# Kernel tuning notes

Hardware: AMD Instinct MI355X
Metric: run time of the kernel (lower is better)

Reference implementation:

```python
import jax, jax.numpy as jnp
import numpy as np

DIAG = 64          # dynamic_mask_scale: |i-j| >= DIAG is masked
NEG_INF = float('-inf')

def _band_mask(L, diagonal):
    # True where masked out: j >= i + diagonal or i >= j + diagonal  <=>  |i-j| >= diagonal
    i = jnp.arange(L)[:, None]
    j = jnp.arange(L)[None, :]
    return jnp.abs(i - j) >= diagonal  # [L, L] bool

def setup_inputs() -> dict:
    key = jax.random.key(0)
    k1, k2, k3, k4 = jax.random.split(key, 4)
    B, L, H, E = 2, 2048, 8, 64
    queries = jax.random.normal(k1, (B, L, H, E), dtype=jnp.float32)
    keys = jax.random.normal(k2, (B, L, H, E), dtype=jnp.float32)
    values = jax.random.normal(k3, (B, L, H, E), dtype=jnp.float32)
    sigma = jax.random.normal(k4, (B, L, H), dtype=jnp.float32)
    attn_mask = jnp.zeros((B, 1, L, L), dtype=bool)  # unused (dynamic mask path)
    return {"queries": queries, "keys": keys, "values": values,
            "sigma": sigma, "attn_mask": attn_mask}

def reference(queries, keys, values, sigma, attn_mask):
    B, L, H, E = queries.shape
    scale = 1.0 / jnp.sqrt(jnp.float32(E))
    # scores: [B, H, L, S]
    scores = jnp.einsum('blhe,bshe->bhls', queries, keys)
    mask = _band_mask(L, DIAG)  # [L, L]
    scores = jnp.where(mask[None, None, :, :], NEG_INF, scores)
    attn = scale * scores
    series = jax.nn.softmax(attn, axis=-1)  # dropout p=0 -> identity
    V = jnp.einsum('bhls,bshd->blhd', series, values)
    return (V, series)
```

## Files before the change

### kernel.cpp

```cpp
#include <hip/hip_runtime.h>
#include <cstdint>

#define BB    2
#define LL    2048
#define HH    8
#define EE    64
#define DIAG  64
#define BAND  127
#define RR    16
#define TILE  143
#define SK    68
#define NT    256

__global__ __launch_bounds__(NT, 3) void anomaly_attn_kernel(
    const float* __restrict__ Q,
    const float* __restrict__ K,
    const float* __restrict__ V,
    float* __restrict__ outV,
    float* __restrict__ outS)
{
    __shared__ float lds_kv[TILE * SK];
    __shared__ float lds_s[RR * 128];
    __shared__ float lds_q[RR * EE];

    const int bid  = blockIdx.x;
    const int gblk = (bid & 7) * 256 + (bid >> 3);
    const int rb   = gblk & 127;
    const int h    = (gblk >> 7) & 7;
    const int b    = gblk >> 10;
    const int i0   = rb * RR;

    const int t    = threadIdx.x;
    const int wave = t >> 6;
    const int lane = t & 63;

    const size_t headOff = ((size_t)b * LL * HH + h) * EE;
    const int    rowStr  = HH * EE;

    {
        const int qrow = t >> 4, qf = t & 15;
        ((float4*)lds_q)[t] =
            *(const float4*)(Q + headOff + (size_t)(i0 + qrow) * rowStr + qf * 4);

        for (int idx = t; idx < TILE * 16; idx += NT) {
            const int trow = idx >> 4, tf = idx & 15;
            int j = i0 - (DIAG - 1) + trow;
            j = j < 0 ? 0 : (j > LL - 1 ? LL - 1 : j);
            float4 kv = *(const float4*)(K + headOff + (size_t)j * rowStr + tf * 4);
            *(float4*)(lds_kv + trow * SK + tf * 4) = kv;
        }
    }
    __syncthreads();

    const float scale = 0.125f;
    for (int r4 = 0; r4 < 4; ++r4) {
        const int r = wave * 4 + r4;
        const int i = i0 + r;
        const float* qrow = lds_q + r * EE;
        const float* k1   = lds_kv + (r + lane) * SK;
        const float* k2   = k1 + 64 * SK;
        float s1 = 0.f, s2 = 0.f;
#pragma unroll
        for (int c = 0; c < 16; ++c) {
            const float4 q4 = *(const float4*)(qrow + c * 4);
            const float4 a4 = *(const float4*)(k1 + c * 4);
            const float4 b4 = *(const float4*)(k2 + c * 4);
            s1 += q4.x * a4.x + q4.y * a4.y + q4.z * a4.z + q4.w * a4.w;
            s2 += q4.x * b4.x + q4.y * b4.y + q4.z * b4.z + q4.w * b4.w;
        }
        const int  slot2 = lane + 64;
        const bool v1 = (i - (DIAG - 1) + lane) >= 0;
        const bool v2 = (slot2 < BAND) && (i - (DIAG - 1) + slot2 < LL);
        float sc1 = v1 ? s1 * scale : -3.0e38f;
        float sc2 = v2 ? s2 * scale : -3.0e38f;

        float m = fmaxf(sc1, sc2);
#pragma unroll
        for (int off = 1; off < 64; off <<= 1)
            m = fmaxf(m, __shfl_xor(m, off, 64));
        float p1 = v1 ? __expf(sc1 - m) : 0.f;
        float p2 = v2 ? __expf(sc2 - m) : 0.f;
        float l = p1 + p2;
#pragma unroll
        for (int off = 1; off < 64; off <<= 1)
            l += __shfl_xor(l, off, 64);
        const float inv = 1.0f / l;
        lds_s[r * 128 + lane]  = p1 * inv;
        lds_s[r * 128 + slot2] = p2 * inv;
    }
    __syncthreads();

    for (int idx = t; idx < TILE * 16; idx += NT) {
        const int trow = idx >> 4, tf = idx & 15;
        int j = i0 - (DIAG - 1) + trow;
        j = j < 0 ? 0 : (j > LL - 1 ? LL - 1 : j);
        float4 vv = *(const float4*)(V + headOff + (size_t)j * rowStr + tf * 4);
        *(float4*)(lds_kv + trow * SK + tf * 4) = vv;
    }
    __syncthreads();

    for (int r4 = 0; r4 < 4; ++r4) {
        const int r = wave * 4 + r4;
        const int i = i0 + r;
        float4* srow4 = (float4*)(outS + (((size_t)(b * HH + h)) * LL + i) * LL);
        const int start = i - (DIAG - 1);
        const float* sp = lds_s + r * 128;
#pragma unroll
        for (int k = 0; k < 8; ++k) {
            const int col4 = lane + k * 64;
            const int d0   = col4 * 4 - start;
            float4 v = make_float4(0.f, 0.f, 0.f, 0.f);
            if (d0 + 3 >= 0 && d0 <= BAND - 1) {
                int ix = d0;
                int i0c = ix < 0 ? 0 : (ix > 127 ? 127 : ix);
                int i1c = ix + 1 < 0 ? 0 : (ix + 1 > 127 ? 127 : ix + 1);
                int i2c = ix + 2 < 0 ? 0 : (ix + 2 > 127 ? 127 : ix + 2);
                int i3c = ix + 3 < 0 ? 0 : (ix + 3 > 127 ? 127 : ix + 3);
                v.x = (ix     >= 0) ? sp[i0c] : 0.f;
                v.y = (ix + 1 >= 0) ? sp[i1c] : 0.f;
                v.z = (ix + 2 >= 0) ? sp[i2c] : 0.f;
                v.w = (ix + 3 >= 0) ? sp[i3c] : 0.f;
            }
            srow4[col4] = v;
        }
    }

    {
        const int e4   = lane & 15;
        const int jsub = lane >> 4;
        for (int r4 = 0; r4 < 4; ++r4) {
            const int r = wave * 4 + r4;
            const int i = i0 + r;
            const float* sp = lds_s + r * 128;
            float4 acc = make_float4(0.f, 0.f, 0.f, 0.f);
#pragma unroll
            for (int p = 0; p < 32; ++p) {
                const int   slot = p * 4 + jsub;
                const float w    = sp[slot];
                const float4 vv  = *(const float4*)(lds_kv + (r + slot) * SK + e4 * 4);
                acc.x += w * vv.x;
                acc.y += w * vv.y;
                acc.z += w * vv.z;
                acc.w += w * vv.w;
            }
#pragma unroll
            for (int off = 16; off <= 32; off <<= 1) {
                acc.x += __shfl_xor(acc.x, off, 64);
                acc.y += __shfl_xor(acc.y, off, 64);
                acc.z += __shfl_xor(acc.z, off, 64);
                acc.w += __shfl_xor(acc.w, off, 64);
            }
            if (lane < 16)
                ((float4*)(outV + headOff + (size_t)i * rowStr))[e4] = acc;
        }
    }
}

extern "C" void kernel_launch(void* const* d_in, const int* in_sizes, int n_in,
                              void* d_out, int out_size, void* d_ws, size_t ws_size,
                              hipStream_t stream) {
    const float* Q = (const float*)d_in[0];
    const float* K = (const float*)d_in[1];
    const float* V = (const float*)d_in[2];

    float* outV = (float*)d_out;
    float* outS = (float*)d_out + (size_t)BB * LL * HH * EE;

    const int grid = (BB * HH * LL) / RR;
    anomaly_attn_kernel<<<grid, NT, 0, stream>>>(Q, K, V, outV, outS);
}
```

Measured before the change: 346.7 us.

## Share aligned K/V window across rows, zero-fill series early, reuse loads across rows

Switches the key/value tile to one aligned window shared by all 16 rows, starting at i0-64, so each wave computes 4 rows together and reuses each K/V load from LDS across them. The series output is written in two passes: the zero region first, before any compute, and then a compact aligned band copied from a padded LDS buffer with coalesced float4 stores. This replaces the old per-element clamped gather. The aim is fewer LDS reads and better overlap of the large zero-write traffic, at the cost of more registers and some redundant dot products over the wider window.

```diff
diff --git a/kernel.cpp b/kernel.cpp
--- a/kernel.cpp
+++ b/kernel.cpp
@@ -6,10 +6,10 @@
 #define HH    8
 #define EE    64
 #define DIAG  64
-#define BAND  127
 #define RR    16
-#define TILE  143
+#define WCAP  144
 #define SK    68
+#define PSK   148
 #define NT    256
 
 __global__ __launch_bounds__(NT, 3) void anomaly_attn_kernel(
@@ -19,9 +19,9 @@
     float* __restrict__ outV,
     float* __restrict__ outS)
 {
-    __shared__ float lds_kv[TILE * SK];
-    __shared__ float lds_s[RR * 128];
+    __shared__ float lds_kv[WCAP * SK];
     __shared__ float lds_q[RR * EE];
+    __shared__ float lds_p[RR * PSK];
 
     const int bid  = blockIdx.x;
     const int gblk = (bid & 7) * 256 + (bid >> 3);
@@ -37,121 +37,143 @@
     const size_t headOff = ((size_t)b * LL * HH + h) * EE;
     const int    rowStr  = HH * EE;
 
+    const int j0      = i0 - DIAG;
+    const int wstart  = j0 < 0 ? 0 : j0;
+    int       wend    = i0 + 80; if (wend > LL) wend = LL;
+    const int width4  = (wend - wstart) >> 2;
+    const int wstart4 = wstart >> 2;
+    const int zf4     = (LL >> 2) - width4;
+
+    float* srow0 = outS + (((size_t)(b * HH + h)) * LL + i0) * LL;
+
+    {
+        const float4 z = make_float4(0.f, 0.f, 0.f, 0.f);
+        for (int row = 0; row < RR; ++row) {
+            float4* srow4 = (float4*)(srow0 + (size_t)row * LL);
+            for (int c = t; c < zf4; c += NT) {
+                const int col4 = c < wstart4 ? c : c + width4;
+                srow4[col4] = z;
+            }
+        }
+    }
+
     {
         const int qrow = t >> 4, qf = t & 15;
-        ((float4*)lds_q)[t] =
+        *(float4*)(lds_q + qrow * EE + qf * 4) =
             *(const float4*)(Q + headOff + (size_t)(i0 + qrow) * rowStr + qf * 4);
-
-        for (int idx = t; idx < TILE * 16; idx += NT) {
+        for (int idx = t; idx < WCAP * 16; idx += NT) {
             const int trow = idx >> 4, tf = idx & 15;
-            int j = i0 - (DIAG - 1) + trow;
-            j = j < 0 ? 0 : (j > LL - 1 ? LL - 1 : j);
-            float4 kv = *(const float4*)(K + headOff + (size_t)j * rowStr + tf * 4);
-            *(float4*)(lds_kv + trow * SK + tf * 4) = kv;
+            int j = j0 + trow; j = j < 0 ? 0 : (j > LL - 1 ? LL - 1 : j);
+            *(float4*)(lds_kv + trow * SK + tf * 4) =
+                *(const float4*)(K + headOff + (size_t)j * rowStr + tf * 4);
         }
     }
     __syncthreads();
 
-    const float scale = 0.125f;
-    for (int r4 = 0; r4 < 4; ++r4) {
-        const int r = wave * 4 + r4;
-        const int i = i0 + r;
-        const float* qrow = lds_q + r * EE;
-        const float* k1   = lds_kv + (r + lane) * SK;
-        const float* k2   = k1 + 64 * SK;
-        float s1 = 0.f, s2 = 0.f;
+    {
+        float sa[4] = {0,0,0,0}, sb[4] = {0,0,0,0}, sc3[4] = {0,0,0,0};
+        const float* ka = lds_kv + lane * SK;
+        const float* kb = lds_kv + (lane + 64) * SK;
+        const float* kc = lds_kv + (128 + (lane & 15)) * SK;
+        const float* qb = lds_q + wave * 4 * EE;
 #pragma unroll
         for (int c = 0; c < 16; ++c) {
-            const float4 q4 = *(const float4*)(qrow + c * 4);
-            const float4 a4 = *(const float4*)(k1 + c * 4);
-            const float4 b4 = *(const float4*)(k2 + c * 4);
-            s1 += q4.x * a4.x + q4.y * a4.y + q4.z * a4.z + q4.w * a4.w;
-            s2 += q4.x * b4.x + q4.y * b4.y + q4.z * b4.z + q4.w * b4.w;
+            const float4 A  = *(const float4*)(ka + c * 4);
+            const float4 Bv = *(const float4*)(kb + c * 4);
+            const float4 Cv = *(const float4*)(kc + c * 4);
+#pragma unroll
+            for (int r = 0; r < 4; ++r) {
+                const float4 q4 = *(const float4*)(qb + r * EE + c * 4);
+                sa[r]  += q4.x * A.x  + q4.y * A.y  + q4.z * A.z  + q4.w * A.w;
+                sb[r]  += q4.x * Bv.x + q4.y * Bv.y + q4.z * Bv.z + q4.w * Bv.w;
+                sc3[r] += q4.x * Cv.x + q4.y * Cv.y + q4.z * Cv.z + q4.w * Cv.w;
+            }
         }
-        const int  slot2 = lane + 64;
-        const bool v1 = (i - (DIAG - 1) + lane) >= 0;
-        const bool v2 = (slot2 < BAND) && (i - (DIAG - 1) + slot2 < LL);
-        float sc1 = v1 ? s1 * scale : -3.0e38f;
-        float sc2 = v2 ? s2 * scale : -3.0e38f;
+        const float scale = 0.125f;
+#pragma unroll
+        for (int r = 0; r < 4; ++r) {
+            const int rr = wave * 4 + r;
+            const bool va = (lane >= rr + 1) && (j0 + lane >= 0);
+            const bool vb = (lane <= rr + 63) && (i0 + lane < LL);
+            const bool vc = (lane < 16) && (lane <= rr - 1) && (i0 + DIAG + lane < LL);
+            float As = va ? sa[r]  * scale : -3.0e38f;
+            float Bs = vb ? sb[r]  * scale : -3.0e38f;
+            float Cs = vc ? sc3[r] * scale : -3.0e38f;
 
-        float m = fmaxf(sc1, sc2);
+            float m = fmaxf(As, fmaxf(Bs, Cs));
 #pragma unroll
-        for (int off = 1; off < 64; off <<= 1)
-            m = fmaxf(m, __shfl_xor(m, off, 64));
-        float p1 = v1 ? __expf(sc1 - m) : 0.f;
-        float p2 = v2 ? __expf(sc2 - m) : 0.f;
-        float l = p1 + p2;
+            for (int off = 1; off < 64; off <<= 1)
+                m = fmaxf(m, __shfl_xor(m, off, 64));
+            float pa = va ? __expf(As - m) : 0.f;
+            float pb = vb ? __expf(Bs - m) : 0.f;
+            float pc = vc ? __expf(Cs - m) : 0.f;
+            float l = pa + pb + pc;
 #pragma unroll
-        for (int off = 1; off < 64; off <<= 1)
-            l += __shfl_xor(l, off, 64);
-        const float inv = 1.0f / l;
-        lds_s[r * 128 + lane]  = p1 * inv;
-        lds_s[r * 128 + slot2] = p2 * inv;
+            for (int off = 1; off < 64; off <<= 1)
+                l += __shfl_xor(l, off, 64);
+            const float inv = 1.0f / l;
+            lds_p[rr * PSK + lane]       = pa * inv;
+            lds_p[rr * PSK + 64 + lane]  = pb * inv;
+            if (lane < 16)
+                lds_p[rr * PSK + 128 + lane] = pc * inv;
+        }
     }
     __syncthreads();
 
-    for (int idx = t; idx < TILE * 16; idx += NT) {
+    {
+        const int woff4 = wstart4 - (j0 >> 2);
+        const int total = RR * width4;
+        for (int idx = t; idx < total; idx += NT) {
+            const int row = idx / width4;
+            const int c   = idx - row * width4;
+            const float4 v = *(const float4*)(lds_p + row * PSK + (woff4 + c) * 4);
+            ((float4*)(srow0 + (size_t)row * LL))[wstart4 + c] = v;
+        }
+    }
+
+    for (int idx = t; idx < WCAP * 16; idx += NT) {
         const int trow = idx >> 4, tf = idx & 15;
-        int j = i0 - (DIAG - 1) + trow;
-        j = j < 0 ? 0 : (j > LL - 1 ? LL - 1 : j);
-        float4 vv = *(const float4*)(V + headOff + (size_t)j * rowStr + tf * 4);
-        *(float4*)(lds_kv + trow * SK + tf * 4) = vv;
+        int j = j0 + trow; j = j < 0 ? 0 : (j > LL - 1 ? LL - 1 : j);
+        *(float4*)(lds_kv + trow * SK + tf * 4) =
+            *(const float4*)(V + headOff + (size_t)j * rowStr + tf * 4);
     }
     __syncthreads();
-
-    for (int r4 = 0; r4 < 4; ++r4) {
-        const int r = wave * 4 + r4;
-        const int i = i0 + r;
-        float4* srow4 = (float4*)(outS + (((size_t)(b * HH + h)) * LL + i) * LL);
-        const int start = i - (DIAG - 1);
-        const float* sp = lds_s + r * 128;
-#pragma unroll
-        for (int k = 0; k < 8; ++k) {
-            const int col4 = lane + k * 64;
-            const int d0   = col4 * 4 - start;
-            float4 v = make_float4(0.f, 0.f, 0.f, 0.f);
-            if (d0 + 3 >= 0 && d0 <= BAND - 1) {
-                int ix = d0;
-                int i0c = ix < 0 ? 0 : (ix > 127 ? 127 : ix);
-                int i1c = ix + 1 < 0 ? 0 : (ix + 1 > 127 ? 127 : ix + 1);
-                int i2c = ix + 2 < 0 ? 0 : (ix + 2 > 127 ? 127 : ix + 2);
-                int i3c = ix + 3 < 0 ? 0 : (ix + 3 > 127 ? 127 : ix + 3);
-                v.x = (ix     >= 0) ? sp[i0c] : 0.f;
-                v.y = (ix + 1 >= 0) ? sp[i1c] : 0.f;
-                v.z = (ix + 2 >= 0) ? sp[i2c] : 0.f;
-                v.w = (ix + 3 >= 0) ? sp[i3c] : 0.f;
-            }
-            srow4[col4] = v;
-        }
-    }
 
     {
         const int e4   = lane & 15;
         const int jsub = lane >> 4;
-        for (int r4 = 0; r4 < 4; ++r4) {
-            const int r = wave * 4 + r4;
-            const int i = i0 + r;
-            const float* sp = lds_s + r * 128;
-            float4 acc = make_float4(0.f, 0.f, 0.f, 0.f);
+        float4 a0 = make_float4(0,0,0,0), a1 = a0, a2 = a0, a3 = a0;
+        const float* pr = lds_p + (wave * 4) * PSK;
 #pragma unroll
-            for (int p = 0; p < 32; ++p) {
-                const int   slot = p * 4 + jsub;
-                const float w    = sp[slot];
-                const float4 vv  = *(const float4*)(lds_kv + (r + slot) * SK + e4 * 4);
-                acc.x += w * vv.x;
-                acc.y += w * vv.y;
-                acc.z += w * vv.z;
-                acc.w += w * vv.w;
-            }
+        for (int k = 0; k < WCAP / 4; ++k) {
+            const int jrel = jsub + 4 * k;
+            const float4 vv = *(const float4*)(lds_kv + jrel * SK + e4 * 4);
+            const float w0 = pr[jrel];
+            const float w1 = pr[PSK + jrel];
+            const float w2 = pr[2 * PSK + jrel];
+            const float w3 = pr[3 * PSK + jrel];
+            a0.x += w0 * vv.x; a0.y += w0 * vv.y; a0.z += w0 * vv.z; a0.w += w0 * vv.w;
+            a1.x += w1 * vv.x; a1.y += w1 * vv.y; a1.z += w1 * vv.z; a1.w += w1 * vv.w;
+            a2.x += w2 * vv.x; a2.y += w2 * vv.y; a2.z += w2 * vv.z; a2.w += w2 * vv.w;
+            a3.x += w3 * vv.x; a3.y += w3 * vv.y; a3.z += w3 * vv.z; a3.w += w3 * vv.w;
+        }
 #pragma unroll
-            for (int off = 16; off <= 32; off <<= 1) {
-                acc.x += __shfl_xor(acc.x, off, 64);
-                acc.y += __shfl_xor(acc.y, off, 64);
-                acc.z += __shfl_xor(acc.z, off, 64);
-                acc.w += __shfl_xor(acc.w, off, 64);
-            }
-            if (lane < 16)
-                ((float4*)(outV + headOff + (size_t)i * rowStr))[e4] = acc;
+        for (int off = 16; off <= 32; off <<= 1) {
+            a0.x += __shfl_xor(a0.x, off, 64); a0.y += __shfl_xor(a0.y, off, 64);
+            a0.z += __shfl_xor(a0.z, off, 64); a0.w += __shfl_xor(a0.w, off, 64);
+            a1.x += __shfl_xor(a1.x, off, 64); a1.y += __shfl_xor(a1.y, off, 64);
+            a1.z += __shfl_xor(a1.z, off, 64); a1.w += __shfl_xor(a1.w, off, 64);
+            a2.x += __shfl_xor(a2.x, off, 64); a2.y += __shfl_xor(a2.y, off, 64);
+            a2.z += __shfl_xor(a2.z, off, 64); a2.w += __shfl_xor(a2.w, off, 64);
+            a3.x += __shfl_xor(a3.x, off, 64); a3.y += __shfl_xor(a3.y, off, 64);
+            a3.z += __shfl_xor(a3.z, off, 64); a3.w += __shfl_xor(a3.w, off, 64);
+        }
+        if (lane < 16) {
+            float4* o0 = (float4*)(outV + headOff + (size_t)(i0 + wave * 4 + 0) * rowStr);
+            float4* o1 = (float4*)(outV + headOff + (size_t)(i0 + wave * 4 + 1) * rowStr);
+            float4* o2 = (float4*)(outV + headOff + (size_t)(i0 + wave * 4 + 2) * rowStr);
+            float4* o3 = (float4*)(outV + headOff + (size_t)(i0 + wave * 4 + 3) * rowStr);
+            o0[e4] = a0; o1[e4] = a1; o2[e4] = a2; o3[e4] = a3;
         }
     }
 }
```

Measured after the change: 607.3 us. 75.2% more time.
